# Performance work log

Hardware: AMD Instinct MI355X
Metric: run time of the kernel (lower is better)

## Reference

```python
import jax, jax.numpy as jnp
import numpy as np

D_MODEL = 1024
N_HEAD = 16
T = 2048
HEAD = D_MODEL // N_HEAD  # 64
RANKS = [32, 16, 8, 8]
BLOCKS = [2048, 1024, 512, 256]  # seq_len // 2**i ('default')
OFFS = np.cumsum([0] + RANKS)


def setup_inputs() -> dict:
    key = jax.random.key(0)
    k0, k1, k2 = jax.random.split(key, 3)
    s = 0.02
    x = jax.random.normal(k0, (1, T, D_MODEL), dtype=jnp.float32)
    W_attn = jax.random.normal(k1, (D_MODEL, 3 * D_MODEL), dtype=jnp.float32) * s
    b_attn = jnp.zeros((3 * D_MODEL,), dtype=jnp.float32)
    W_proj = jax.random.normal(k2, (D_MODEL, D_MODEL), dtype=jnp.float32) * s
    b_proj = jnp.zeros((D_MODEL,), dtype=jnp.float32)
    return {"x": x, "W_attn": W_attn, "b_attn": b_attn, "W_proj": W_proj, "b_proj": b_proj}


def reference(x, W_attn, b_attn, W_proj, b_proj):
    B = x.shape[0]
    qkv = x @ W_attn + b_attn  # (B,T,3*D)
    q, k, v = jnp.split(qkv, 3, axis=-1)
    # (B,H,T,HEAD)
    q = q.reshape(B, T, N_HEAD, HEAD).transpose(0, 2, 1, 3)
    k = k.reshape(B, T, N_HEAD, HEAD).transpose(0, 2, 1, 3)
    v = v.reshape(B, T, N_HEAD, HEAD).transpose(0, 2, 1, 3)

    att = jnp.zeros((B, N_HEAD, T, T), dtype=x.dtype)
    for i, (bdx, r) in enumerate(zip(BLOCKS, RANKS)):
        nb = T // bdx
        qi = q[..., OFFS[i]:OFFS[i + 1]].reshape(B, N_HEAD, nb, bdx, r)
        ki = k[..., OFFS[i]:OFFS[i + 1]].reshape(B, N_HEAD, nb, bdx, r)
        blk = jnp.einsum('bhnir,bhnjr->bhnij', qi, ki) * (1.0 / r)  # (B,H,nb,bdx,bdx)
        # scatter block-diagonal scores into full T x T matrix
        att5 = att.reshape(B, N_HEAD, nb, bdx, nb, bdx)
        ar = jnp.arange(nb)
        att5 = att5.at[:, :, ar, :, ar, :].add(jnp.moveaxis(blk, 2, 0))
        att = att5.reshape(B, N_HEAD, T, T)

    causal = jnp.tril(jnp.ones((T, T), dtype=bool))
    att = jnp.where(causal, att, -jnp.inf)
    att = jax.nn.softmax(att, axis=-1)
    y = att @ v  # (B,H,T,HEAD)
    y = y.transpose(0, 2, 1, 3).reshape(B, T, D_MODEL)
    return y @ W_proj + b_proj
```

## Files before the change

kernel.cpp:

```cpp
#include <hip/hip_runtime.h>

using bf16x8 = __attribute__((ext_vector_type(8))) short;
using u16x8  = __attribute__((ext_vector_type(8))) unsigned short;
using f32x4  = __attribute__((ext_vector_type(4))) float;

#define DEVI __device__ __forceinline__

DEVI unsigned short f2bf(float f) {
  union { float ff; unsigned u; } v; v.ff = f;
  unsigned r = v.u + 0x7FFFu + ((v.u >> 16) & 1u);
  return (unsigned short)(r >> 16);
}

DEVI float bf2f(unsigned short s) {
  union { unsigned u; float f; } t; t.u = ((unsigned)s) << 16;
  return t.f;
}

DEVI int cvtpk(float lo, float hi) {
  int r;
  asm("v_cvt_pk_bf16_f32 %0, %1, %2" : "=v"(r) : "v"(lo), "v"(hi));
  return r;
}

DEVI void g2l16(const void* g, void* l) {
  __builtin_amdgcn_global_load_lds(
      (const __attribute__((address_space(1))) unsigned int*)g,
      (__attribute__((address_space(3))) unsigned int*)l, 16, 0, 0);
}

__global__ __launch_bounds__(256) void k_prep(
    const float* __restrict__ x, const float* __restrict__ Wa, const float* __restrict__ Wp,
    unsigned short* __restrict__ xb, unsigned short* __restrict__ WaT,
    unsigned short* __restrict__ WpT) {
  __shared__ float tile[32][33];
  const int b = blockIdx.x;
  const int tid = threadIdx.x;
  if (b < 2048) {
    const int i = b * 256 + tid;
    float4 v = reinterpret_cast<const float4*>(x)[i];
    ushort4 o;
    o.x = f2bf(v.x); o.y = f2bf(v.y); o.z = f2bf(v.z); o.w = f2bf(v.w);
    reinterpret_cast<ushort4*>(xb)[i] = o;
    return;
  }
  const float* in;
  unsigned short* out;
  int c0, r0, C;
  if (b < 5120) {
    const int bb = b - 2048;
    in = Wa; out = WaT; C = 3072;
    c0 = (bb % 96) * 32; r0 = (bb / 96) * 32;
  } else {
    const int bb = b - 5120;
    in = Wp; out = WpT; C = 1024;
    c0 = (bb & 31) * 32; r0 = (bb >> 5) * 32;
  }
  const int xx = tid & 31, yy = tid >> 5;
  for (int i = yy; i < 32; i += 8) tile[i][xx] = in[(size_t)(r0 + i) * C + c0 + xx];
  __syncthreads();
  for (int i = yy; i < 32; i += 8) out[(size_t)(c0 + i) * 1024 + r0 + xx] = f2bf(tile[xx][i]);
}

__global__ __launch_bounds__(256) void k_gemm_qkv(
    const unsigned short* __restrict__ A, const unsigned short* __restrict__ Bt,
    const float* __restrict__ bias,
    unsigned short* __restrict__ qs, unsigned short* __restrict__ kbuf,
    unsigned short* __restrict__ vT) {
  constexpr int K = 1024;
  __shared__ __align__(16) unsigned short As[2][128 * 64];
  __shared__ __align__(16) unsigned short Bs[2][64 * 64];
  const int lane = threadIdx.x & 63, wid = threadIdx.x >> 6;
  const int m0 = blockIdx.y * 128, n0 = blockIdx.x * 64;
  const int wr = (wid >> 1) * 64, wc = (wid & 1) * 32;
  const int g = lane >> 4, li = lane & 15;
  f32x4 acc[4][2] = {};

#define STAGE_QKV(buf, k0)                                                              \
  {                                                                                     \
    _Pragma("unroll")                                                                   \
    for (int c = wid * 4; c < wid * 4 + 4; c++) {                                       \
      const int flat = c * 1024 + lane * 16;                                            \
      const int row = flat >> 7, colb = flat & 127;                                     \
      g2l16((const char*)A + ((size_t)(m0 + row) * K + (k0)) * 2 + colb,                \
            (char*)As[buf] + c * 1024);                                                 \
    }                                                                                   \
    _Pragma("unroll")                                                                   \
    for (int c = wid * 2; c < wid * 2 + 2; c++) {                                       \
      const int flat = c * 1024 + lane * 16;                                            \
      const int row = flat >> 7, colb = flat & 127;                                     \
      g2l16((const char*)Bt + ((size_t)(n0 + row) * K + (k0)) * 2 + colb,               \
            (char*)Bs[buf] + c * 1024);                                                 \
    }                                                                                   \
  }

  STAGE_QKV(0, 0);
  __syncthreads();
  int buf = 0;
  for (int t = 0; t < 16; t++) {
    if (t < 15) STAGE_QKV(buf ^ 1, (t + 1) * 64);
#pragma unroll
    for (int ks = 0; ks < 2; ks++) {
      const int kk = ks * 32 + g * 8;
      bf16x8 a[4], b[2];
#pragma unroll
      for (int i = 0; i < 4; i++)
        a[i] = *reinterpret_cast<const bf16x8*>(As[buf] + (wr + i * 16 + li) * 64 + kk);
#pragma unroll
      for (int j = 0; j < 2; j++)
        b[j] = *reinterpret_cast<const bf16x8*>(Bs[buf] + (wc + j * 16 + li) * 64 + kk);
#pragma unroll
      for (int i = 0; i < 4; i++)
#pragma unroll
        for (int j = 0; j < 2; j++)
          acc[i][j] = __builtin_amdgcn_mfma_f32_16x16x32_bf16(a[i], b[j], acc[i][j], 0, 0, 0);
    }
    __syncthreads();
    buf ^= 1;
  }

  const int rb = m0 + wr + g * 4;
  const int cb = n0 + wc + li;
#pragma unroll
  for (int j = 0; j < 2; j++) {
    const int c = cb + j * 16;
    const float bv = bias[c];
    const int hq = c >> 6, d = c & 63;
    const float sc = d < 32 ? 0.03125f : (d < 48 ? 0.0625f : 0.125f);
#pragma unroll
    for (int i = 0; i < 4; i++) {
#pragma unroll
      for (int r = 0; r < 4; r++) {
        const int t = rb + i * 16 + r;
        const float val = acc[i][j][r] + bv;
        if (c < 1024) {
          qs[((size_t)(hq * 2048 + t) << 6) + d] = f2bf(val * sc);
        } else if (c < 2048) {
          kbuf[((size_t)((hq - 16) * 2048 + t) << 6) + d] = f2bf(val);
        } else {
          vT[(size_t)((hq - 32) * 64 + d) * 2048 + t] = f2bf(val);
        }
      }
    }
  }
#undef STAGE_QKV
}

DEVI int chunk_off(int qt) {
  const int off[17] = {0,1,2,3,4,6,8,10,12,15,18,21,24,28,32,36,40};
  return off[qt];
}

__global__ __launch_bounds__(256) void k_attn_part(
    const unsigned short* __restrict__ qs, const unsigned short* __restrict__ kbuf,
    const unsigned short* __restrict__ vT,
    unsigned short* __restrict__ o_part, float* __restrict__ ml) {
  __shared__ __align__(16) unsigned short Ks[2][128 * 64];
  __shared__ __align__(16) unsigned short Vs[2][64 * 128];
  const int lane = threadIdx.x & 63, wid = threadIdx.x >> 6;
  const int g = lane >> 4, li = lane & 15;

  const int h = blockIdx.x / 40;
  const int rem = blockIdx.x % 40;
  int qt = 0;
#pragma unroll
  for (int i = 0; i < 16; i++)
    if (rem >= chunk_off(i + 1)) qt = i + 1;
  const int ci = rem - chunk_off(qt);
  const int kt0 = ci * 4;
  const int kt1 = min(qt, kt0 + 3);
  const int q0 = qt * 128;

  const bf16x8 bzero = {0, 0, 0, 0, 0, 0, 0, 0};

#define STAGE_KV(buf, kt)                                                               \
  for (int c = wid; c < 16; c += 4) {                                                   \
    const int fb = c * 1024;                                                            \
    const int flat = fb + lane * 16;                                                    \
    {                                                                                   \
      const int row = flat >> 7;                                                        \
      const int cs = (((flat >> 4) & 7) ^ (row & 7)) << 4;                              \
      g2l16((const char*)kbuf + (((size_t)(h * 2048 + (kt) * 128 + row)) << 7) + cs,    \
            (char*)Ks[buf] + fb);                                                       \
    }                                                                                   \
    {                                                                                   \
      const int row = flat >> 8;                                                        \
      const int cs = (((flat >> 4) & 15) ^ (row & 15)) << 4;                            \
      g2l16((const char*)vT + ((size_t)(h * 64 + row) * 2048 + (kt) * 128) * 2 + cs,    \
            (char*)Vs[buf] + fb);                                                       \
    }                                                                                   \
  }

  bf16x8 qf[2][2];
#pragma unroll
  for (int mi = 0; mi < 2; mi++)
#pragma unroll
    for (int ks = 0; ks < 2; ks++) {
      const int t = q0 + wid * 32 + mi * 16 + li;
      const int d = ks * 32 + g * 8;
      qf[mi][ks] = *reinterpret_cast<const bf16x8*>(qs + ((size_t)(h * 2048 + t) << 6) + d);
    }

  f32x4 o[2][4] = {};
  float m_run[2] = {-1e30f, -1e30f}, l_run[2] = {0.f, 0.f};

  const int q256 = qt >> 1;
  STAGE_KV(0, kt0);
  int buf = 0;
  for (int kt = kt0; kt <= kt1; kt++) {
    __syncthreads();
    if (kt < kt1) STAGE_KV(buf ^ 1, kt + 1);

    const int x = q256 ^ (kt >> 1);
    const int Keff = (x == 0) ? 64 : ((x >= 4) ? 32 : ((x >= 2) ? 48 : 56));

    f32x4 st[8][2] = {};
    __builtin_amdgcn_s_setprio(1);
#pragma unroll
    for (int cf = 0; cf < 8; cf++) {
      const int krow = cf * 16 + li;
      const bf16x8 a0 = *reinterpret_cast<const bf16x8*>(
          Ks[buf] + krow * 64 + ((g ^ (krow & 7)) << 3));
      st[cf][0] = __builtin_amdgcn_mfma_f32_16x16x32_bf16(a0, qf[0][0], st[cf][0], 0, 0, 0);
      st[cf][1] = __builtin_amdgcn_mfma_f32_16x16x32_bf16(a0, qf[1][0], st[cf][1], 0, 0, 0);
    }
    if (Keff > 32) {
      const bool zf = (32 + g * 8) >= Keff;
#pragma unroll
      for (int cf = 0; cf < 8; cf++) {
        const int krow = cf * 16 + li;
        bf16x8 a1 = *reinterpret_cast<const bf16x8*>(
            Ks[buf] + krow * 64 + (((4 + g) ^ (krow & 7)) << 3));
        if (zf) a1 = bzero;
        st[cf][0] = __builtin_amdgcn_mfma_f32_16x16x32_bf16(a1, qf[0][1], st[cf][0], 0, 0, 0);
        st[cf][1] = __builtin_amdgcn_mfma_f32_16x16x32_bf16(a1, qf[1][1], st[cf][1], 0, 0, 0);
      }
    }
    __builtin_amdgcn_s_setprio(0);

    if (kt == qt) {
#pragma unroll
      for (int cf = 0; cf < 8; cf++)
#pragma unroll
        for (int mi = 0; mi < 2; mi++)
#pragma unroll
          for (int r = 0; r < 4; r++) {
            const int t2 = cf * 16 + g * 4 + r;
            const int qq = wid * 32 + mi * 16 + li;
            if (t2 > qq) st[cf][mi][r] = -1e30f;
          }
    }

    int pk[2][8][2];
    float corrb[2][4];
#pragma unroll
    for (int mi = 0; mi < 2; mi++) {
      float c4[8];
#pragma unroll
      for (int cf = 0; cf < 8; cf++)
        c4[cf] = fmaxf(fmaxf(st[cf][mi][0], st[cf][mi][1]),
                       fmaxf(st[cf][mi][2], st[cf][mi][3]));
      const float ta = fmaxf(fmaxf(c4[0], c4[1]), fmaxf(c4[2], c4[3]));
      const float tb = fmaxf(fmaxf(c4[4], c4[5]), fmaxf(c4[6], c4[7]));
      float tm = fmaxf(ta, tb);
      tm = fmaxf(tm, __shfl_xor(tm, 16));
      tm = fmaxf(tm, __shfl_xor(tm, 32));
      const float mn = fmaxf(m_run[mi], tm);
      const float corr = __expf(m_run[mi] - mn);
      m_run[mi] = mn;
      float sum = 0.f;
#pragma unroll
      for (int cf = 0; cf < 8; cf++) {
        const float p0 = __expf(st[cf][mi][0] - mn);
        const float p1 = __expf(st[cf][mi][1] - mn);
        const float p2 = __expf(st[cf][mi][2] - mn);
        const float p3 = __expf(st[cf][mi][3] - mn);
        sum += (p0 + p1) + (p2 + p3);
        pk[mi][cf][0] = cvtpk(p0, p1);
        pk[mi][cf][1] = cvtpk(p2, p3);
      }
      sum += __shfl_xor(sum, 16);
      sum += __shfl_xor(sum, 32);
      l_run[mi] = l_run[mi] * corr + sum;
      corrb[mi][0] = __shfl(corr, 4 * g + 0);
      corrb[mi][1] = __shfl(corr, 4 * g + 1);
      corrb[mi][2] = __shfl(corr, 4 * g + 2);
      corrb[mi][3] = __shfl(corr, 4 * g + 3);
    }
#pragma unroll
    for (int mi = 0; mi < 2; mi++)
#pragma unroll
      for (int nf = 0; nf < 4; nf++)
#pragma unroll
        for (int r = 0; r < 4; r++)
          o[mi][nf][r] *= corrb[mi][r];

    __builtin_amdgcn_s_setprio(1);
#pragma unroll
    for (int ks2 = 0; ks2 < 4; ks2++) {
      bf16x8 pa[2];
#pragma unroll
      for (int mi = 0; mi < 2; mi++) {
        union { int i[4]; bf16x8 v; } u;
        u.i[0] = pk[mi][2 * ks2][0];
        u.i[1] = pk[mi][2 * ks2][1];
        u.i[2] = pk[mi][2 * ks2 + 1][0];
        u.i[3] = pk[mi][2 * ks2 + 1][1];
        pa[mi] = u.v;
      }
      bf16x8 vb[4];
#pragma unroll
      for (int nf = 0; nf < 4; nf++) {
        const int vrow = nf * 16 + li;
        const int rm = vrow & 15;
        const int ch0 = 4 * ks2 + (g >> 1);
        const int b8 = (g & 1) * 8;
        union { struct { int2 lo, hi; } p; bf16x8 v; } u;
        u.p.lo = *reinterpret_cast<const int2*>(
            (const char*)Vs[buf] + vrow * 256 + (((ch0 + 0) ^ rm) << 4) + b8);
        u.p.hi = *reinterpret_cast<const int2*>(
            (const char*)Vs[buf] + vrow * 256 + (((ch0 + 2) ^ rm) << 4) + b8);
        vb[nf] = u.v;
      }
#pragma unroll
      for (int mi = 0; mi < 2; mi++)
#pragma unroll
        for (int nf = 0; nf < 4; nf++)
          o[mi][nf] = __builtin_amdgcn_mfma_f32_16x16x32_bf16(pa[mi], vb[nf], o[mi][nf], 0, 0, 0);
    }
    __builtin_amdgcn_s_setprio(0);
    buf ^= 1;
  }
#undef STAGE_KV

  const size_t pbase = (size_t)blockIdx.x * 8192;
#pragma unroll
  for (int mi = 0; mi < 2; mi++) {
#pragma unroll
    for (int nf = 0; nf < 4; nf++)
#pragma unroll
      for (int r = 0; r < 4; r++) {
        const int row = wid * 32 + mi * 16 + g * 4 + r;
        o_part[pbase + (size_t)row * 64 + nf * 16 + li] = f2bf(o[mi][nf][r]);
      }
  }
  if (g == 0) {
#pragma unroll
    for (int mi = 0; mi < 2; mi++) {
      const int row = wid * 32 + mi * 16 + li;
      ml[(size_t)blockIdx.x * 256 + row] = m_run[mi];
      ml[(size_t)blockIdx.x * 256 + 128 + row] = l_run[mi];
    }
  }
}

__global__ __launch_bounds__(256) void k_combine(
    const unsigned short* __restrict__ o_part, const float* __restrict__ ml,
    unsigned short* __restrict__ yb) {
  const int h = blockIdx.x >> 4, qt = blockIdx.x & 15;
  const int nc = (qt >> 2) + 1;
  const int base = h * 40 + chunk_off(qt);
  const int row = threadIdx.x >> 1;
  const int c0 = (threadIdx.x & 1) * 32;

  float m_i[4], l_i[4];
  float M = -1e30f;
  for (int ci = 0; ci < nc; ci++) {
    m_i[ci] = ml[(size_t)(base + ci) * 256 + row];
    l_i[ci] = ml[(size_t)(base + ci) * 256 + 128 + row];
    M = fmaxf(M, m_i[ci]);
  }
  float L = 0.f, w[4];
  for (int ci = 0; ci < nc; ci++) {
    w[ci] = __expf(m_i[ci] - M);
    L += w[ci] * l_i[ci];
  }
  const float inv = 1.0f / L;

  float acc[32];
#pragma unroll
  for (int j = 0; j < 32; j++) acc[j] = 0.f;
  for (int ci = 0; ci < nc; ci++) {
    const u16x8* src = reinterpret_cast<const u16x8*>(
        o_part + (size_t)(base + ci) * 8192 + (size_t)row * 64 + c0);
    const float wc = w[ci];
#pragma unroll
    for (int j8 = 0; j8 < 4; j8++) {
      u16x8 v = src[j8];
#pragma unroll
      for (int e = 0; e < 8; e++) acc[j8 * 8 + e] += wc * bf2f(v[e]);
    }
  }
  const int t = qt * 128 + row;
  unsigned short* dst = yb + (size_t)t * 1024 + h * 64 + c0;
#pragma unroll
  for (int j8 = 0; j8 < 4; j8++) {
    ushort4 pk;
    pk.x = f2bf(acc[j8 * 8 + 0] * inv);
    pk.y = f2bf(acc[j8 * 8 + 1] * inv);
    pk.z = f2bf(acc[j8 * 8 + 2] * inv);
    pk.w = f2bf(acc[j8 * 8 + 3] * inv);
    ushort4 pk2;
    pk2.x = f2bf(acc[j8 * 8 + 4] * inv);
    pk2.y = f2bf(acc[j8 * 8 + 5] * inv);
    pk2.z = f2bf(acc[j8 * 8 + 6] * inv);
    pk2.w = f2bf(acc[j8 * 8 + 7] * inv);
    reinterpret_cast<ushort4*>(dst)[j8 * 2 + 0] = pk;
    reinterpret_cast<ushort4*>(dst)[j8 * 2 + 1] = pk2;
  }
}

__global__ __launch_bounds__(256) void k_gemm_proj(
    const unsigned short* __restrict__ A, const unsigned short* __restrict__ Bt,
    const float* __restrict__ bias, float* __restrict__ out) {
  constexpr int K = 1024;
  __shared__ __align__(16) unsigned short As[2][64 * 64];
  __shared__ __align__(16) unsigned short Bs[2][64 * 64];
  const int lane = threadIdx.x & 63, wid = threadIdx.x >> 6;
  const int m0 = blockIdx.y * 64, n0 = blockIdx.x * 64;
  const int wr = (wid >> 1) * 32, wc = (wid & 1) * 32;
  const int g = lane >> 4, li = lane & 15;
  f32x4 acc[2][2] = {};

#define STAGE_PROJ(buf, k0)                                                             \
  {                                                                                     \
    _Pragma("unroll")                                                                   \
    for (int c = wid * 2; c < wid * 2 + 2; c++) {                                       \
      const int flat = c * 1024 + lane * 16;                                            \
      const int row = flat >> 7, colb = flat & 127;                                     \
      g2l16((const char*)A + ((size_t)(m0 + row) * K + (k0)) * 2 + colb,                \
            (char*)As[buf] + c * 1024);                                                 \
      g2l16((const char*)Bt + ((size_t)(n0 + row) * K + (k0)) * 2 + colb,               \
            (char*)Bs[buf] + c * 1024);                                                 \
    }                                                                                   \
  }

  STAGE_PROJ(0, 0);
  __syncthreads();
  int buf = 0;
  for (int t = 0; t < 16; t++) {
    if (t < 15) STAGE_PROJ(buf ^ 1, (t + 1) * 64);
#pragma unroll
    for (int ks = 0; ks < 2; ks++) {
      const int kk = ks * 32 + g * 8;
      bf16x8 a[2], b[2];
#pragma unroll
      for (int i = 0; i < 2; i++)
        a[i] = *reinterpret_cast<const bf16x8*>(As[buf] + (wr + i * 16 + li) * 64 + kk);
#pragma unroll
      for (int j = 0; j < 2; j++)
        b[j] = *reinterpret_cast<const bf16x8*>(Bs[buf] + (wc + j * 16 + li) * 64 + kk);
#pragma unroll
      for (int i = 0; i < 2; i++)
#pragma unroll
        for (int j = 0; j < 2; j++)
          acc[i][j] = __builtin_amdgcn_mfma_f32_16x16x32_bf16(a[i], b[j], acc[i][j], 0, 0, 0);
    }
    __syncthreads();
    buf ^= 1;
  }

  const int rb = m0 + wr + g * 4;
  const int cb = n0 + wc + li;
#pragma unroll
  for (int j = 0; j < 2; j++) {
    const int c = cb + j * 16;
    const float bv = bias[c];
#pragma unroll
    for (int i = 0; i < 2; i++) {
#pragma unroll
      for (int r = 0; r < 4; r++) {
        const int t = rb + i * 16 + r;
        out[(size_t)t * 1024 + c] = acc[i][j][r] + bv;
      }
    }
  }
#undef STAGE_PROJ
}

extern "C" void kernel_launch(void* const* d_in, const int* in_sizes, int n_in,
                              void* d_out, int out_size, void* d_ws, size_t ws_size,
                              hipStream_t stream) {
  const float* x      = (const float*)d_in[0];
  const float* W_attn = (const float*)d_in[1];
  const float* b_attn = (const float*)d_in[2];
  const float* W_proj = (const float*)d_in[3];
  const float* b_proj = (const float*)d_in[4];
  float* out = (float*)d_out;
  char* ws = (char*)d_ws;
  const size_t MB = 1024 * 1024;
  unsigned short* xb  = (unsigned short*)(ws + 0 * MB);
  unsigned short* WaT = (unsigned short*)(ws + 4 * MB);
  unsigned short* WpT = (unsigned short*)(ws + 10 * MB);
  unsigned short* qs  = (unsigned short*)(ws + 12 * MB);
  unsigned short* kb  = (unsigned short*)(ws + 16 * MB);
  unsigned short* vT  = (unsigned short*)(ws + 20 * MB);
  unsigned short* yb  = (unsigned short*)(ws + 24 * MB);
  unsigned short* o_part = (unsigned short*)(ws + 28 * MB);
  float* ml     = (float*)(ws + 39 * MB);

  k_prep<<<dim3(6144), dim3(256), 0, stream>>>(x, W_attn, W_proj, xb, WaT, WpT);
  k_gemm_qkv<<<dim3(48, 16), dim3(256), 0, stream>>>(xb, WaT, b_attn, qs, kb, vT);
  k_attn_part<<<dim3(640), dim3(256), 0, stream>>>(qs, kb, vT, o_part, ml);
  k_combine<<<dim3(256), dim3(256), 0, stream>>>(o_part, ml, yb);
  k_gemm_proj<<<dim3(16, 32), dim3(256), 0, stream>>>(yb, WpT, b_proj, out);
}
```

Before: 96.52 us.

## Use exp2 softmax with lazy rescale, direct output for short rows, vectorized V stores

Folds log2(e) into the Q scaling so the softmax can use exp2f. The running max is updated only when a row's new max exceeds the old one by more than a threshold, which skips most of the rescale multiplies. Query tiles with a single key chunk (qt<4) now normalize and write straight to yb, so the combine kernel only handles the remaining tiles. The QKV epilogue is split by region with packed ushort4 stores for vT, and the prep transpose converts to bf16 before the shared-memory staging. The lazy rescale lets unnormalized values grow by up to 2^12 before correction, which relies on fp32 and bf16 range.

```diff
diff --git a/kernel.cpp b/kernel.cpp
--- a/kernel.cpp
+++ b/kernel.cpp
@@ -5,6 +5,8 @@
 using f32x4  = __attribute__((ext_vector_type(4))) float;
 
 #define DEVI __device__ __forceinline__
+
+#define LOG2E 1.4426950408889634f
 
 DEVI unsigned short f2bf(float f) {
   union { float ff; unsigned u; } v; v.ff = f;
@@ -33,7 +35,7 @@
     const float* __restrict__ x, const float* __restrict__ Wa, const float* __restrict__ Wp,
     unsigned short* __restrict__ xb, unsigned short* __restrict__ WaT,
     unsigned short* __restrict__ WpT) {
-  __shared__ float tile[32][33];
+  __shared__ unsigned short tile[32][33];
   const int b = blockIdx.x;
   const int tid = threadIdx.x;
   if (b < 2048) {
@@ -57,9 +59,9 @@
     c0 = (bb & 31) * 32; r0 = (bb >> 5) * 32;
   }
   const int xx = tid & 31, yy = tid >> 5;
-  for (int i = yy; i < 32; i += 8) tile[i][xx] = in[(size_t)(r0 + i) * C + c0 + xx];
+  for (int i = yy; i < 32; i += 8) tile[i][xx] = f2bf(in[(size_t)(r0 + i) * C + c0 + xx]);
   __syncthreads();
-  for (int i = yy; i < 32; i += 8) out[(size_t)(c0 + i) * 1024 + r0 + xx] = f2bf(tile[xx][i]);
+  for (int i = yy; i < 32; i += 8) out[(size_t)(c0 + i) * 1024 + r0 + xx] = tile[xx][i];
 }
 
 __global__ __launch_bounds__(256) void k_gemm_qkv(
@@ -121,25 +123,47 @@
 
   const int rb = m0 + wr + g * 4;
   const int cb = n0 + wc + li;
-#pragma unroll
-  for (int j = 0; j < 2; j++) {
-    const int c = cb + j * 16;
-    const float bv = bias[c];
-    const int hq = c >> 6, d = c & 63;
-    const float sc = d < 32 ? 0.03125f : (d < 48 ? 0.0625f : 0.125f);
-#pragma unroll
-    for (int i = 0; i < 4; i++) {
-#pragma unroll
-      for (int r = 0; r < 4; r++) {
-        const int t = rb + i * 16 + r;
-        const float val = acc[i][j][r] + bv;
-        if (c < 1024) {
-          qs[((size_t)(hq * 2048 + t) << 6) + d] = f2bf(val * sc);
-        } else if (c < 2048) {
-          kbuf[((size_t)((hq - 16) * 2048 + t) << 6) + d] = f2bf(val);
-        } else {
-          vT[(size_t)((hq - 32) * 64 + d) * 2048 + t] = f2bf(val);
-        }
+  const int region = n0 >> 10;
+  if (region == 0) {
+#pragma unroll
+    for (int j = 0; j < 2; j++) {
+      const int c = cb + j * 16;
+      const float bv = bias[c];
+      const int hq = c >> 6, d = c & 63;
+      const float sc = (d < 32 ? 0.03125f : (d < 48 ? 0.0625f : 0.125f)) * LOG2E;
+#pragma unroll
+      for (int i = 0; i < 4; i++)
+#pragma unroll
+        for (int r = 0; r < 4; r++)
+          qs[((size_t)(hq * 2048 + rb + i * 16 + r) << 6) + d] = f2bf((acc[i][j][r] + bv) * sc);
+    }
+  } else if (region == 1) {
+#pragma unroll
+    for (int j = 0; j < 2; j++) {
+      const int c = cb + j * 16;
+      const float bv = bias[c];
+      const int hq = (c >> 6) - 16, d = c & 63;
+#pragma unroll
+      for (int i = 0; i < 4; i++)
+#pragma unroll
+        for (int r = 0; r < 4; r++)
+          kbuf[((size_t)(hq * 2048 + rb + i * 16 + r) << 6) + d] = f2bf(acc[i][j][r] + bv);
+    }
+  } else {
+#pragma unroll
+    for (int j = 0; j < 2; j++) {
+      const int c = cb + j * 16;
+      const float bv = bias[c];
+      const int row = c - 2048;
+#pragma unroll
+      for (int i = 0; i < 4; i++) {
+        const int t0 = rb + i * 16;
+        ushort4 pk;
+        pk.x = f2bf(acc[i][j][0] + bv);
+        pk.y = f2bf(acc[i][j][1] + bv);
+        pk.z = f2bf(acc[i][j][2] + bv);
+        pk.w = f2bf(acc[i][j][3] + bv);
+        *reinterpret_cast<ushort4*>(vT + (size_t)row * 2048 + t0) = pk;
       }
     }
   }
@@ -154,7 +178,8 @@
 __global__ __launch_bounds__(256) void k_attn_part(
     const unsigned short* __restrict__ qs, const unsigned short* __restrict__ kbuf,
     const unsigned short* __restrict__ vT,
-    unsigned short* __restrict__ o_part, float* __restrict__ ml) {
+    unsigned short* __restrict__ o_part, float* __restrict__ ml,
+    unsigned short* __restrict__ yb) {
   __shared__ __align__(16) unsigned short Ks[2][128 * 64];
   __shared__ __align__(16) unsigned short Vs[2][64 * 128];
   const int lane = threadIdx.x & 63, wid = threadIdx.x >> 6;
@@ -252,7 +277,6 @@
     }
 
     int pk[2][8][2];
-    float corrb[2][4];
 #pragma unroll
     for (int mi = 0; mi < 2; mi++) {
       float c4[8];
@@ -265,35 +289,37 @@
       float tm = fmaxf(ta, tb);
       tm = fmaxf(tm, __shfl_xor(tm, 16));
       tm = fmaxf(tm, __shfl_xor(tm, 32));
-      const float mn = fmaxf(m_run[mi], tm);
-      const float corr = __expf(m_run[mi] - mn);
-      m_run[mi] = mn;
+      if (!__all(tm <= m_run[mi] + 12.0f)) {
+        const float mn = fmaxf(m_run[mi], tm);
+        const float corr = exp2f(m_run[mi] - mn);
+        m_run[mi] = mn;
+        l_run[mi] *= corr;
+        float cb0 = __shfl(corr, 4 * g + 0);
+        float cb1 = __shfl(corr, 4 * g + 1);
+        float cb2 = __shfl(corr, 4 * g + 2);
+        float cb3 = __shfl(corr, 4 * g + 3);
+#pragma unroll
+        for (int nf = 0; nf < 4; nf++) {
+          o[mi][nf][0] *= cb0; o[mi][nf][1] *= cb1;
+          o[mi][nf][2] *= cb2; o[mi][nf][3] *= cb3;
+        }
+      }
+      const float mn = m_run[mi];
       float sum = 0.f;
 #pragma unroll
       for (int cf = 0; cf < 8; cf++) {
-        const float p0 = __expf(st[cf][mi][0] - mn);
-        const float p1 = __expf(st[cf][mi][1] - mn);
-        const float p2 = __expf(st[cf][mi][2] - mn);
-        const float p3 = __expf(st[cf][mi][3] - mn);
+        const float p0 = exp2f(st[cf][mi][0] - mn);
+        const float p1 = exp2f(st[cf][mi][1] - mn);
+        const float p2 = exp2f(st[cf][mi][2] - mn);
+        const float p3 = exp2f(st[cf][mi][3] - mn);
         sum += (p0 + p1) + (p2 + p3);
         pk[mi][cf][0] = cvtpk(p0, p1);
         pk[mi][cf][1] = cvtpk(p2, p3);
       }
       sum += __shfl_xor(sum, 16);
       sum += __shfl_xor(sum, 32);
-      l_run[mi] = l_run[mi] * corr + sum;
-      corrb[mi][0] = __shfl(corr, 4 * g + 0);
-      corrb[mi][1] = __shfl(corr, 4 * g + 1);
-      corrb[mi][2] = __shfl(corr, 4 * g + 2);
-      corrb[mi][3] = __shfl(corr, 4 * g + 3);
-    }
-#pragma unroll
-    for (int mi = 0; mi < 2; mi++)
-#pragma unroll
-      for (int nf = 0; nf < 4; nf++)
-#pragma unroll
-        for (int r = 0; r < 4; r++)
-          o[mi][nf][r] *= corrb[mi][r];
+      l_run[mi] += sum;
+    }
 
     __builtin_amdgcn_s_setprio(1);
 #pragma unroll
@@ -333,6 +359,26 @@
   }
 #undef STAGE_KV
 
+  if (qt < 4) {
+#pragma unroll
+    for (int mi = 0; mi < 2; mi++) {
+      const float inv = 1.0f / l_run[mi];
+      float ib[4];
+      ib[0] = __shfl(inv, 4 * g + 0);
+      ib[1] = __shfl(inv, 4 * g + 1);
+      ib[2] = __shfl(inv, 4 * g + 2);
+      ib[3] = __shfl(inv, 4 * g + 3);
+#pragma unroll
+      for (int nf = 0; nf < 4; nf++)
+#pragma unroll
+        for (int r = 0; r < 4; r++) {
+          const int t = q0 + wid * 32 + mi * 16 + g * 4 + r;
+          yb[(size_t)t * 1024 + h * 64 + nf * 16 + li] = f2bf(o[mi][nf][r] * ib[r]);
+        }
+    }
+    return;
+  }
+
   const size_t pbase = (size_t)blockIdx.x * 8192;
 #pragma unroll
   for (int mi = 0; mi < 2; mi++) {
@@ -357,7 +403,7 @@
 __global__ __launch_bounds__(256) void k_combine(
     const unsigned short* __restrict__ o_part, const float* __restrict__ ml,
     unsigned short* __restrict__ yb) {
-  const int h = blockIdx.x >> 4, qt = blockIdx.x & 15;
+  const int h = blockIdx.x / 12, qt = blockIdx.x % 12 + 4;
   const int nc = (qt >> 2) + 1;
   const int base = h * 40 + chunk_off(qt);
   const int row = threadIdx.x >> 1;
@@ -372,7 +418,7 @@
   }
   float L = 0.f, w[4];
   for (int ci = 0; ci < nc; ci++) {
-    w[ci] = __expf(m_i[ci] - M);
+    w[ci] = exp2f(m_i[ci] - M);
     L += w[ci] * l_i[ci];
   }
   const float inv = 1.0f / L;
@@ -501,7 +547,7 @@
 
   k_prep<<<dim3(6144), dim3(256), 0, stream>>>(x, W_attn, W_proj, xb, WaT, WpT);
   k_gemm_qkv<<<dim3(48, 16), dim3(256), 0, stream>>>(xb, WaT, b_attn, qs, kb, vT);
-  k_attn_part<<<dim3(640), dim3(256), 0, stream>>>(qs, kb, vT, o_part, ml);
-  k_combine<<<dim3(256), dim3(256), 0, stream>>>(o_part, ml, yb);
+  k_attn_part<<<dim3(640), dim3(256), 0, stream>>>(qs, kb, vT, o_part, ml, yb);
+  k_combine<<<dim3(192), dim3(256), 0, stream>>>(o_part, ml, yb);
   k_gemm_proj<<<dim3(16, 32), dim3(256), 0, stream>>>(yb, WpT, b_proj, out);
 }
```

New measurement: 96.94 us. About the same (+0.4%).
